# Kernel optimization log

Hardware: AMD Instinct MI355X
Metric: run time of the kernel (lower is better)

The kernel has to match this reference:

```python
import jax, jax.numpy as jnp
import numpy as np

DIM, M, K = 768, 48, 256
MK = M * K            # 12288
H = MK // 2           # 6144
MID = int(0.75 * MK)  # 9216
B = 2048
MIN_DIST_FACTOR = 10.0
LN_EPS = 1e-5


def setup_inputs() -> dict:
    key = jax.random.key(0)
    ks = jax.random.split(key, 18)
    s = 0.02  # keep exp(sigma_logits) tame
    return {
        "x": jax.random.normal(ks[0], (B, DIM), jnp.float32),
        "codebook": jax.random.normal(ks[1], (M, K, DIM // M), jnp.float32),
        "rot1": jnp.eye(DIM) + s * jax.random.normal(ks[2], (DIM, DIM), jnp.float32),
        "ln_g": jnp.ones((DIM,), jnp.float32),
        "ln_b": jnp.zeros((DIM,), jnp.float32),
        "l1_w": s * jax.random.normal(ks[3], (MID, DIM), jnp.float32),
        "l1_b": jnp.zeros((MID,), jnp.float32),
        "mu_w": s * jax.random.normal(ks[4], (H, MID), jnp.float32),
        "mu_b": jnp.zeros((H,), jnp.float32),
        "sig_w": s * jax.random.normal(ks[5], (H, MID), jnp.float32),
        "sig_b": jnp.zeros((H,), jnp.float32),
        "rot2": jnp.eye(H) + s * jax.random.normal(ks[6], (H, H), jnp.float32),
        "l2_w": s * jax.random.normal(ks[7], (MK, H), jnp.float32),
        "l2_b": jnp.zeros((MK,), jnp.float32),
        "interp_param": jax.random.normal(ks[8], (1,), jnp.float32),
        "vae_noise": jax.random.normal(ks[9], (B, H), jnp.float32),
        "gumbel_noise": -jnp.log(-jnp.log(
            jax.random.uniform(ks[10], (B, M, K), jnp.float32, 1e-10, 1.0))),
    }


def _layernorm(x, g, b):
    mu = jnp.mean(x, axis=-1, keepdims=True)
    var = jnp.mean((x - mu) ** 2, axis=-1, keepdims=True)
    return (x - mu) * jax.lax.rsqrt(var + LN_EPS) * g + b


def reference(x, codebook, rot1, ln_g, ln_b, l1_w, l1_b, mu_w, mu_b,
              sig_w, sig_b, rot2, l2_w, l2_b, interp_param,
              vae_noise, gumbel_noise):
    x_rot = x @ rot1.T                                   # [B, DIM]
    xn = _layernorm(x_rot, ln_g, ln_b)
    h1 = jax.nn.relu(xn @ l1_w.T + l1_b)                 # [B, MID]
    mu = h1 @ mu_w.T + mu_b                              # [B, H]
    sigma = jnp.exp(h1 @ sig_w.T + sig_b)                # [B, H]
    z = mu + sigma * vae_noise                           # reparameterized sample
    h = jnp.tanh(z)
    h_rot = h @ rot2.T                                   # [B, H]
    a = jax.nn.relu(h_rot @ l2_w.T + l2_b)               # [B, MK]
    a_r = a.reshape(-1, M, K)                            # [B, M, K]
    # PQ distances: [B, M, 1, d] vs [1, M, K, d] -> [B, M, K]
    d = DIM // M
    xs = x_rot.reshape(-1, M, 1, d)
    cs = codebook.reshape(1, M, K, d)
    dist = jnp.sum((cs - xs) ** 2, axis=-1)
    min_dist = jax.nn.one_hot(jnp.argmin(dist, axis=-1), K, dtype=jnp.float32)
    interp = jax.nn.sigmoid(interp_param[0])
    logits = (1.0 - interp) * a_r + interp * MIN_DIST_FACTOR * min_dist
    # hard gumbel-softmax, tau=1
    y_soft = jax.nn.softmax(logits + gumbel_noise, axis=-1)
    y_hard = jax.nn.one_hot(jnp.argmax(y_soft, axis=-1), K, dtype=y_soft.dtype)
    s = y_hard - jax.lax.stop_gradient(y_soft) + y_soft
    return s
```

## Files before the change

### kernel.cpp

```cpp
#include <hip/hip_runtime.h>
#include <cstddef>
#include <cstdint>

constexpr int kDIM = 768;
constexpr int kM   = 48;
constexpr int kK   = 256;
constexpr int kB   = 2048;
constexpr int kMID = 9216;
constexpr int kH   = 6144;
constexpr int kMK  = 12288;

using bf8v  = __attribute__((ext_vector_type(8))) short;
using f32x4 = __attribute__((ext_vector_type(4))) float;
using s8v   = __attribute__((ext_vector_type(8))) short;

template<bool HASBIAS, int EPI, typename OUT_T>
__global__ __launch_bounds__(256)
void gemm_nt_acc64(const float* __restrict__ A, const float* __restrict__ W,
                   const float* __restrict__ bias, OUT_T* C,
                   const float* zslog, const float* __restrict__ znoise,
                   int N, int Kd)
{
  __shared__ float As[16][132];
  __shared__ float Bs[16][132];
  const int tid  = (int)threadIdx.x;
  const int row0 = (int)blockIdx.y * 128;
  const int col0 = (int)blockIdx.x * 128;
  const int ty = tid >> 4, tx = tid & 15;
  const int i0 = ty * 8, j0 = tx * 8;
  const int fi1 = tid >> 2;
  const int fi2 = fi1 + 64;
  const int kc  = (tid & 3) * 4;

  const float* Ap1 = A + (size_t)(row0 + fi1) * Kd + kc;
  const float* Ap2 = A + (size_t)(row0 + fi2) * Kd + kc;
  const float* Wp1 = W + (size_t)(col0 + fi1) * Kd + kc;
  const float* Wp2 = W + (size_t)(col0 + fi2) * Kd + kc;

  double acc[8][8];
#pragma unroll
  for (int r = 0; r < 8; ++r)
#pragma unroll
    for (int c = 0; c < 8; ++c) acc[r][c] = 0.0;

  for (int kt = 0; kt < Kd; kt += 16) {
    const float4 a1 = *(const float4*)(Ap1 + kt);
    const float4 a2 = *(const float4*)(Ap2 + kt);
    const float4 b1 = *(const float4*)(Wp1 + kt);
    const float4 b2 = *(const float4*)(Wp2 + kt);
    As[kc + 0][fi1] = a1.x; As[kc + 1][fi1] = a1.y; As[kc + 2][fi1] = a1.z; As[kc + 3][fi1] = a1.w;
    As[kc + 0][fi2] = a2.x; As[kc + 1][fi2] = a2.y; As[kc + 2][fi2] = a2.z; As[kc + 3][fi2] = a2.w;
    Bs[kc + 0][fi1] = b1.x; Bs[kc + 1][fi1] = b1.y; Bs[kc + 2][fi1] = b1.z; Bs[kc + 3][fi1] = b1.w;
    Bs[kc + 0][fi2] = b2.x; Bs[kc + 1][fi2] = b2.y; Bs[kc + 2][fi2] = b2.z; Bs[kc + 3][fi2] = b2.w;
    __syncthreads();
#pragma unroll
    for (int kk = 0; kk < 16; ++kk) {
      const float4 av0 = *(const float4*)&As[kk][i0];
      const float4 av1 = *(const float4*)&As[kk][i0 + 4];
      const float4 bv0 = *(const float4*)&Bs[kk][j0];
      const float4 bv1 = *(const float4*)&Bs[kk][j0 + 4];
      const float ar[8] = {av0.x, av0.y, av0.z, av0.w, av1.x, av1.y, av1.z, av1.w};
      const float br[8] = {bv0.x, bv0.y, bv0.z, bv0.w, bv1.x, bv1.y, bv1.z, bv1.w};
      double bd[8];
#pragma unroll
      for (int c = 0; c < 8; ++c) bd[c] = (double)br[c];
#pragma unroll
      for (int r = 0; r < 8; ++r) {
        const double ad = (double)ar[r];
#pragma unroll
        for (int c = 0; c < 8; ++c)
          acc[r][c] = fma(ad, bd[c], acc[r][c]);
      }
    }
    __syncthreads();
  }

  double bvv[8];
#pragma unroll
  for (int c = 0; c < 8; ++c) bvv[c] = 0.0;
  if (HASBIAS) {
#pragma unroll
    for (int c = 0; c < 8; ++c) bvv[c] = (double)bias[col0 + j0 + c];
  }

#pragma unroll
  for (int r = 0; r < 8; ++r) {
    const size_t gbase = (size_t)(row0 + i0 + r) * N + col0 + j0;
    double o[8];
#pragma unroll
    for (int c = 0; c < 8; ++c) {
      double v = acc[r][c];
      if (HASBIAS) v += bvv[c];
      if (EPI == 1) v = fmax(v, 0.0);
      if (EPI == 2) {
        const double sg = exp((double)zslog[gbase + c]);
        v = tanh(v + sg * (double)znoise[gbase + c]);
      }
      o[c] = v;
    }
    if constexpr (sizeof(OUT_T) == 4) {
      float* dst = (float*)C + gbase;
      ((float4*)dst)[0] = make_float4((float)o[0], (float)o[1], (float)o[2], (float)o[3]);
      ((float4*)dst)[1] = make_float4((float)o[4], (float)o[5], (float)o[6], (float)o[7]);
    } else {
      double* dst = (double*)C + gbase;
#pragma unroll
      for (int c = 0; c < 8; ++c) dst[c] = o[c];
    }
  }
}

__device__ __forceinline__ unsigned short bf16rn(float f) {
  const unsigned u = __float_as_uint(f);
  return (unsigned short)((u + 0x7FFFu + ((u >> 16) & 1u)) >> 16);
}

__global__ __launch_bounds__(256)
void split3_k(const float* __restrict__ in, short* __restrict__ out, size_t n)
{
  const size_t i = ((size_t)blockIdx.x * 256 + threadIdx.x) * 8;
  const float4 v0 = *(const float4*)(in + i);
  const float4 v1 = *(const float4*)(in + i + 4);
  const float f[8] = {v0.x, v0.y, v0.z, v0.w, v1.x, v1.y, v1.z, v1.w};
  s8v o1, o2, o3;
#pragma unroll
  for (int j = 0; j < 8; ++j) {
    const unsigned short b1 = bf16rn(f[j]);
    const float r1 = f[j] - __uint_as_float((unsigned)b1 << 16);
    const unsigned short b2 = bf16rn(r1);
    const float r2 = r1 - __uint_as_float((unsigned)b2 << 16);
    const unsigned short b3 = bf16rn(r2);
    o1[j] = (short)b1; o2[j] = (short)b2; o3[j] = (short)b3;
  }
  *(s8v*)(out + i)         = o1;
  *(s8v*)(out + n + i)     = o2;
  *(s8v*)(out + 2 * n + i) = o3;
}

#define GLL16(SRC, DST) __builtin_amdgcn_global_load_lds( \
    (const __attribute__((address_space(1))) void*)(SRC), \
    (__attribute__((address_space(3))) void*)(DST), 16, 0, 0)

template<bool HASBIAS, bool RELU>
__global__ __launch_bounds__(256, 2)
void gemm3_bf16(const short* __restrict__ A3, const short* __restrict__ W3,
                const float* __restrict__ bias, float* __restrict__ C,
                int N, int Kd, int nbx)
{
  __shared__ short lds[6][4096];
  short* smem = &lds[0][0];
  const char* smemc = (const char*)smem;

  int wg = (int)blockIdx.x;
  const int nwg = (int)gridDim.x;
  if ((nwg & 7) == 0) { const int q = nwg >> 3; wg = (wg & 7) * q + (wg >> 3); }
  const int nby = kB / 128;
  const int by = wg % nby, bx = wg / nby;
  const int row0 = by * 128, col0 = bx * 128;

  const int tid = (int)threadIdx.x;
  const int l = tid & 63, w = tid >> 6;
  const int wr = (w & 1) * 64, wc = (w >> 1) * 64;

  const size_t planeAB = (size_t)2048 * Kd * 2;
  const size_t planeWB = (size_t)N * Kd * 2;
  const char* A3b = (const char*)A3;
  const char* W3b = (const char*)W3;

  const int su = 2 * w;
  const int r0 = su * 16 + (l >> 2), r1 = r0 + 16;
  const int q0 = (((l & 3) ^ (r0 & 3)) << 4);
  const int q1 = (((l & 3) ^ (r1 & 3)) << 4);
  const size_t offA0 = (size_t)(row0 + r0) * Kd * 2 + q0;
  const size_t offA1 = (size_t)(row0 + r1) * Kd * 2 + q1;
  const size_t offW0 = (size_t)(col0 + r0) * Kd * 2 + q0;
  const size_t offW1 = (size_t)(col0 + r1) * Kd * 2 + q1;
  short* dA0 = smem + (su + 0) * 512;
  short* dA1 = smem + (su + 1) * 512;

  int aoff[3][4], boff[3][4];
#pragma unroll
  for (int p = 0; p < 3; ++p) {
#pragma unroll
    for (int t = 0; t < 4; ++t) {
      const int Ra = wr + t * 16 + (l & 15);
      aoff[p][t] = p * 8192 + Ra * 64 + ((((l >> 4) << 4)) ^ ((Ra & 3) << 4));
      const int Rb = wc + t * 16 + (l & 15);
      boff[p][t] = (3 + p) * 8192 + Rb * 64 + ((((l >> 4) << 4)) ^ ((Rb & 3) << 4));
    }
  }

  f32x4 acc[4][4];
#pragma unroll
  for (int i = 0; i < 4; ++i)
#pragma unroll
    for (int j = 0; j < 4; ++j) acc[i][j] = f32x4{0.f, 0.f, 0.f, 0.f};

  for (int kt = 0; kt < Kd; kt += 32) {
    const size_t kb = (size_t)kt * 2;
#pragma unroll
    for (int t = 0; t < 3; ++t) {
      GLL16(A3b + t * planeAB + offA0 + kb, dA0 + t * 4096);
      GLL16(A3b + t * planeAB + offA1 + kb, dA1 + t * 4096);
    }
#pragma unroll
    for (int t = 0; t < 3; ++t) {
      GLL16(W3b + t * planeWB + offW0 + kb, dA0 + (3 + t) * 4096);
      GLL16(W3b + t * planeWB + offW1 + kb, dA1 + (3 + t) * 4096);
    }
    __syncthreads();

    bf8v af[3][4], bf_[3][4];
#pragma unroll
    for (int p = 0; p < 3; ++p)
#pragma unroll
      for (int t = 0; t < 4; ++t) {
        af[p][t]  = *(const bf8v*)(smemc + aoff[p][t]);
        bf_[p][t] = *(const bf8v*)(smemc + boff[p][t]);
      }
#pragma unroll
    for (int tr = 0; tr < 4; ++tr)
#pragma unroll
      for (int tc = 0; tc < 4; ++tc) {
        f32x4 c = acc[tr][tc];
        c = __builtin_amdgcn_mfma_f32_16x16x32_bf16(af[0][tr], bf_[0][tc], c, 0, 0, 0);
        c = __builtin_amdgcn_mfma_f32_16x16x32_bf16(af[0][tr], bf_[1][tc], c, 0, 0, 0);
        c = __builtin_amdgcn_mfma_f32_16x16x32_bf16(af[1][tr], bf_[0][tc], c, 0, 0, 0);
        c = __builtin_amdgcn_mfma_f32_16x16x32_bf16(af[0][tr], bf_[2][tc], c, 0, 0, 0);
        c = __builtin_amdgcn_mfma_f32_16x16x32_bf16(af[2][tr], bf_[0][tc], c, 0, 0, 0);
        c = __builtin_amdgcn_mfma_f32_16x16x32_bf16(af[1][tr], bf_[1][tc], c, 0, 0, 0);
        acc[tr][tc] = c;
      }
    __syncthreads();
  }

#pragma unroll
  for (int tc = 0; tc < 4; ++tc) {
    const int colg = col0 + wc + tc * 16 + (l & 15);
    float bv = 0.f;
    if (HASBIAS) bv = bias[colg];
#pragma unroll
    for (int tr = 0; tr < 4; ++tr) {
      const int rowg0 = row0 + wr + tr * 16 + ((l >> 4) << 2);
#pragma unroll
      for (int g = 0; g < 4; ++g) {
        float v = acc[tr][tc][g];
        if (HASBIAS) v += bv;
        if (RELU)    v = fmaxf(v, 0.f);
        C[(size_t)(rowg0 + g) * N + colg] = v;
      }
    }
  }
}

__global__ __launch_bounds__(256)
void layernorm_k(const double* __restrict__ in, const float* __restrict__ g,
                 const float* __restrict__ b, float* __restrict__ out)
{
  const int row = (int)blockIdx.x;
  const int tid = (int)threadIdx.x;
  const double* x = in + (size_t)row * kDIM;
  const double v0 = x[tid], v1 = x[tid + 256], v2 = x[tid + 512];
  __shared__ double red[8];
  double s = v0 + v1 + v2;
#pragma unroll
  for (int off = 32; off; off >>= 1) s += __shfl_xor(s, off);
  if ((tid & 63) == 0) red[tid >> 6] = s;
  __syncthreads();
  const double mean = (red[0] + red[1] + red[2] + red[3]) * (1.0 / 768.0);
  const double d0 = v0 - mean, d1 = v1 - mean, d2 = v2 - mean;
  double q = d0 * d0 + d1 * d1 + d2 * d2;
#pragma unroll
  for (int off = 32; off; off >>= 1) q += __shfl_xor(q, off);
  if ((tid & 63) == 0) red[4 + (tid >> 6)] = q;
  __syncthreads();
  const double var = (red[4] + red[5] + red[6] + red[7]) * (1.0 / 768.0);
  const double rs = 1.0 / sqrt(var + 1e-5);
  float* y = out + (size_t)row * kDIM;
  y[tid]       = (float)(d0 * rs * (double)g[tid]       + (double)b[tid]);
  y[tid + 256] = (float)(d1 * rs * (double)g[tid + 256] + (double)b[tid + 256]);
  y[tid + 512] = (float)(d2 * rs * (double)g[tid + 512] + (double)b[tid + 512]);
}

__global__ __launch_bounds__(256)
void zh_k(const float* __restrict__ mu, float* slog_h, const float* __restrict__ noise)
{
  const size_t i = (size_t)blockIdx.x * 256 + threadIdx.x;
  const double z = (double)mu[i] + exp((double)slog_h[i]) * (double)noise[i];
  slog_h[i] = (float)tanh(z);
}

__global__ __launch_bounds__(256)
void mindist_k(const double* __restrict__ xrot, const float* __restrict__ cb,
               int* __restrict__ minidx)
{
  const int wid  = (int)blockIdx.x * 4 + ((int)threadIdx.x >> 6);
  const int lane = (int)threadIdx.x & 63;
  const int bi = wid / kM, mi = wid % kM;
  const double* xv = xrot + (size_t)bi * kDIM + mi * 16;
  double xs[16];
#pragma unroll
  for (int d = 0; d < 16; ++d) xs[d] = xv[d];
  const float* cm = cb + (size_t)mi * (kK * 16);
  double best = 1e300; int bidx = 0;
#pragma unroll
  for (int j = 0; j < 4; ++j) {
    const int k = lane * 4 + j;
    const float* ck = cm + k * 16;
    double s = 0.0;
#pragma unroll
    for (int d = 0; d < 16; ++d) {
      const double t = (double)ck[d] - xs[d];
      s = fma(t, t, s);
    }
    if (s < best) { best = s; bidx = k; }
  }
#pragma unroll
  for (int off = 32; off; off >>= 1) {
    const double ob = __shfl_xor(best, off);
    const int    oi = __shfl_xor(bidx, off);
    if (ob < best || (ob == best && oi < bidx)) { best = ob; bidx = oi; }
  }
  if (lane == 0) minidx[wid] = bidx;
}

__global__ __launch_bounds__(256)
void finalize_k(float* a, const float* __restrict__ gumbel,
                const int* __restrict__ minidx, const float* __restrict__ interp_param)
{
  const int wid  = (int)blockIdx.x * 4 + ((int)threadIdx.x >> 6);
  const int lane = (int)threadIdx.x & 63;
  const double interp = 1.0 / (1.0 + exp(-(double)interp_param[0]));
  const double w = 1.0 - interp;
  const double bonus = interp * 10.0;
  const int mi = minidx[wid];
  const size_t base = (size_t)wid * 256 + lane * 4;
  const float4 av = *(const float4*)&a[base];
  const float4 gv = *(const float4*)&gumbel[base];
  const int k0 = lane * 4;
  double lg[4] = {w * (double)av.x + (double)gv.x,
                  w * (double)av.y + (double)gv.y,
                  w * (double)av.z + (double)gv.z,
                  w * (double)av.w + (double)gv.w};
#pragma unroll
  for (int j = 0; j < 4; ++j)
    if (k0 + j == mi) lg[j] += bonus;

  double best = -1e300; int bk = 0;
#pragma unroll
  for (int j = 0; j < 4; ++j)
    if (lg[j] > best) { best = lg[j]; bk = k0 + j; }
#pragma unroll
  for (int off = 32; off; off >>= 1) {
    const double ob = __shfl_xor(best, off);
    const int    oi = __shfl_xor(bk, off);
    if (ob > best || (ob == best && oi < bk)) { best = ob; bk = oi; }
  }
  float4 o;
  o.x = (k0 + 0 == bk) ? 1.f : 0.f;
  o.y = (k0 + 1 == bk) ? 1.f : 0.f;
  o.z = (k0 + 2 == bk) ? 1.f : 0.f;
  o.w = (k0 + 3 == bk) ? 1.f : 0.f;
  *(float4*)&a[base] = o;
}

extern "C" void kernel_launch(void* const* d_in, const int* in_sizes, int n_in,
                              void* d_out, int out_size, void* d_ws, size_t ws_size,
                              hipStream_t stream)
{
  const float* x      = (const float*)d_in[0];
  const float* cb     = (const float*)d_in[1];
  const float* rot1   = (const float*)d_in[2];
  const float* ln_g   = (const float*)d_in[3];
  const float* ln_b   = (const float*)d_in[4];
  const float* l1_w   = (const float*)d_in[5];
  const float* l1_b   = (const float*)d_in[6];
  const float* mu_w   = (const float*)d_in[7];
  const float* mu_b   = (const float*)d_in[8];
  const float* sig_w  = (const float*)d_in[9];
  const float* sig_b  = (const float*)d_in[10];
  const float* rot2   = (const float*)d_in[11];
  const float* l2_w   = (const float*)d_in[12];
  const float* l2_b   = (const float*)d_in[13];
  const float* interp = (const float*)d_in[14];
  const float* noise  = (const float*)d_in[15];
  const float* gumb   = (const float*)d_in[16];

  const dim3 blk(256);
  float* aout = (float*)d_out;

  const size_t nXrot = (size_t)kB * kDIM;
  const size_t nH1   = (size_t)kB * kMID;
  const size_t nHH   = (size_t)kB * kH;
  const size_t NEED  = nXrot * 8 + nXrot * 4 + nH1 * 4 + nHH * 4 + nHH * 4
                     + nH1 * 3 * 2 + (size_t)kMK * kH * 3 * 2 + (size_t)kB * kM * 4;

  if (ws_size >= NEED) {
    char* p = (char*)d_ws;
    double* x_rotd = (double*)p;              p += nXrot * 8;
    float*  xn     = (float*)p;               p += nXrot * 4;
    float*  h1     = (float*)p;               p += nH1 * 4;
    float*  mu     = (float*)p;               p += nHH * 4;
    float*  slog   = (float*)p;               p += nHH * 4;
    short*  As3    = (short*)p;               p += nH1 * 3 * 2;
    short*  Ws3    = (short*)p;               p += (size_t)kMK * kH * 3 * 2;
    int*    midx   = (int*)p;

    gemm_nt_acc64<false, 0, double><<<dim3(kDIM / 128, kB / 128), blk, 0, stream>>>(
        x, rot1, nullptr, x_rotd, nullptr, nullptr, kDIM, kDIM);
    layernorm_k<<<dim3(kB), blk, 0, stream>>>(x_rotd, ln_g, ln_b, xn);
    mindist_k<<<dim3(kB * kM / 4), blk, 0, stream>>>(x_rotd, cb, midx);

    split3_k<<<dim3((unsigned)(nXrot / 2048)), blk, 0, stream>>>(xn, As3, nXrot);
    split3_k<<<dim3((unsigned)((size_t)kMID * kDIM / 2048)), blk, 0, stream>>>(l1_w, Ws3, (size_t)kMID * kDIM);
    gemm3_bf16<true, true><<<dim3(kMID / 128 * (kB / 128)), blk, 0, stream>>>(
        As3, Ws3, l1_b, h1, kMID, kDIM, kMID / 128);

    split3_k<<<dim3((unsigned)(nH1 / 2048)), blk, 0, stream>>>(h1, As3, nH1);
    split3_k<<<dim3((unsigned)((size_t)kH * kMID / 2048)), blk, 0, stream>>>(mu_w, Ws3, (size_t)kH * kMID);
    gemm3_bf16<true, false><<<dim3(kH / 128 * (kB / 128)), blk, 0, stream>>>(
        As3, Ws3, mu_b, mu, kH, kMID, kH / 128);
    split3_k<<<dim3((unsigned)((size_t)kH * kMID / 2048)), blk, 0, stream>>>(sig_w, Ws3, (size_t)kH * kMID);
    gemm3_bf16<true, false><<<dim3(kH / 128 * (kB / 128)), blk, 0, stream>>>(
        As3, Ws3, sig_b, slog, kH, kMID, kH / 128);

    zh_k<<<dim3((unsigned)(nHH / 256)), blk, 0, stream>>>(mu, slog, noise);

    split3_k<<<dim3((unsigned)(nHH / 2048)), blk, 0, stream>>>(slog, As3, nHH);
    split3_k<<<dim3((unsigned)((size_t)kH * kH / 2048)), blk, 0, stream>>>(rot2, Ws3, (size_t)kH * kH);
    gemm3_bf16<false, false><<<dim3(kH / 128 * (kB / 128)), blk, 0, stream>>>(
        As3, Ws3, nullptr, h1, kH, kH, kH / 128);

    split3_k<<<dim3((unsigned)(nHH / 2048)), blk, 0, stream>>>(h1, As3, nHH);
    split3_k<<<dim3((unsigned)((size_t)kMK * kH / 2048)), blk, 0, stream>>>(l2_w, Ws3, (size_t)kMK * kH);
    gemm3_bf16<true, true><<<dim3(kMK / 128 * (kB / 128)), blk, 0, stream>>>(
        As3, Ws3, l2_b, aout, kMK, kH, kMK / 128);

    finalize_k<<<dim3(kB * kM / 4), blk, 0, stream>>>(aout, gumb, midx, interp);
    return;
  }

  char* wsb    = (char*)d_ws;
  double* x_rotd = (double*)wsb;
  float*  xn     = (float*)(wsb + (size_t)kB * kDIM * 8);
  float*  h1     = xn   + (size_t)kB * kDIM;
  float*  slog   = h1   + (size_t)kB * kMID;
  int*    midx   = (int*)(slog + (size_t)kB * kH);
  float*  hrot   = h1;

  gemm_nt_acc64<false, 0, double><<<dim3(kDIM / 128, kB / 128), blk, 0, stream>>>(
      x, rot1, nullptr, x_rotd, nullptr, nullptr, kDIM, kDIM);
  layernorm_k<<<dim3(kB), blk, 0, stream>>>(x_rotd, ln_g, ln_b, xn);
  mindist_k<<<dim3(kB * kM / 4), blk, 0, stream>>>(x_rotd, cb, midx);
  gemm_nt_acc64<true, 1, float><<<dim3(kMID / 128, kB / 128), blk, 0, stream>>>(
      xn, l1_w, l1_b, h1, nullptr, nullptr, kMID, kDIM);
  gemm_nt_acc64<true, 0, float><<<dim3(kH / 128, kB / 128), blk, 0, stream>>>(
      h1, sig_w, sig_b, slog, nullptr, nullptr, kH, kMID);
  gemm_nt_acc64<true, 2, float><<<dim3(kH / 128, kB / 128), blk, 0, stream>>>(
      h1, mu_w, mu_b, slog, slog, noise, kH, kMID);
  gemm_nt_acc64<false, 0, float><<<dim3(kH / 128, kB / 128), blk, 0, stream>>>(
      slog, rot2, nullptr, hrot, nullptr, nullptr, kH, kH);
  gemm_nt_acc64<true, 1, float><<<dim3(kMK / 128, kB / 128), blk, 0, stream>>>(
      hrot, l2_w, l2_b, aout, nullptr, nullptr, kMK, kH);
  finalize_k<<<dim3(kB * kM / 4), blk, 0, stream>>>(aout, gumb, midx, interp);
}
```

Before: 6.455 ms.

## Double-buffer LDS tiles in split-bf16 GEMM to overlap loads with MFMA

The split-bf16 GEMM now keeps two LDS stages and issues the global-to-LDS loads for the next K-step before running the MFMAs on the current stage. It waits with an explicit vmcnt(0) and a barrier at the end of each iteration, replacing the load-then-sync-then-compute pattern. The LDS swizzle is also changed so the row-dependent XOR uses bits 1-2 of the row. The point is to hide global load latency behind compute. The cost is 96KB of LDS per block, which likely limits occupancy to one block per CU, and the launch-bounds occupancy hint is dropped.

```diff
diff --git a/kernel.cpp b/kernel.cpp
--- a/kernel.cpp
+++ b/kernel.cpp
@@ -13,6 +13,13 @@
 using bf8v  = __attribute__((ext_vector_type(8))) short;
 using f32x4 = __attribute__((ext_vector_type(4))) float;
 using s8v   = __attribute__((ext_vector_type(8))) short;
+
+#define GLL16(SRC, DST) __builtin_amdgcn_global_load_lds( \
+    (const __attribute__((address_space(1))) void*)(SRC), \
+    (__attribute__((address_space(3))) void*)(DST), 16, 0, 0)
+
+#define FENCE() asm volatile("" ::: "memory")
+#define WAITV0() asm volatile("s_waitcnt vmcnt(0)" ::: "memory")
 
 template<bool HASBIAS, int EPI, typename OUT_T>
 __global__ __launch_bounds__(256)
@@ -137,19 +144,13 @@
   *(s8v*)(out + 2 * n + i) = o3;
 }
 
-#define GLL16(SRC, DST) __builtin_amdgcn_global_load_lds( \
-    (const __attribute__((address_space(1))) void*)(SRC), \
-    (__attribute__((address_space(3))) void*)(DST), 16, 0, 0)
-
 template<bool HASBIAS, bool RELU>
-__global__ __launch_bounds__(256, 2)
+__global__ __launch_bounds__(256)
 void gemm3_bf16(const short* __restrict__ A3, const short* __restrict__ W3,
                 const float* __restrict__ bias, float* __restrict__ C,
                 int N, int Kd, int nbx)
 {
-  __shared__ short lds[6][4096];
-  short* smem = &lds[0][0];
-  const char* smemc = (const char*)smem;
+  __shared__ char ldsb[98304];
 
   int wg = (int)blockIdx.x;
   const int nwg = (int)gridDim.x;
@@ -169,14 +170,13 @@
 
   const int su = 2 * w;
   const int r0 = su * 16 + (l >> 2), r1 = r0 + 16;
-  const int q0 = (((l & 3) ^ (r0 & 3)) << 4);
-  const int q1 = (((l & 3) ^ (r1 & 3)) << 4);
-  const size_t offA0 = (size_t)(row0 + r0) * Kd * 2 + q0;
-  const size_t offA1 = (size_t)(row0 + r1) * Kd * 2 + q1;
-  const size_t offW0 = (size_t)(col0 + r0) * Kd * 2 + q0;
-  const size_t offW1 = (size_t)(col0 + r1) * Kd * 2 + q1;
-  short* dA0 = smem + (su + 0) * 512;
-  short* dA1 = smem + (su + 1) * 512;
+  const int qsw = (((l & 3) ^ ((l >> 3) & 3)) << 4);
+  const size_t offA0 = (size_t)(row0 + r0) * Kd * 2 + qsw;
+  const size_t offA1 = (size_t)(row0 + r1) * Kd * 2 + qsw;
+  const size_t offW0 = (size_t)(col0 + r0) * Kd * 2 + qsw;
+  const size_t offW1 = (size_t)(col0 + r1) * Kd * 2 + qsw;
+  const int d0 = su * 1024;
+  const int d1 = d0 + 1024;
 
   int aoff[3][4], boff[3][4];
 #pragma unroll
@@ -184,9 +184,9 @@
 #pragma unroll
     for (int t = 0; t < 4; ++t) {
       const int Ra = wr + t * 16 + (l & 15);
-      aoff[p][t] = p * 8192 + Ra * 64 + ((((l >> 4) << 4)) ^ ((Ra & 3) << 4));
+      aoff[p][t] = p * 8192 + Ra * 64 + ((((l >> 4)) ^ ((Ra >> 1) & 3)) << 4);
       const int Rb = wc + t * 16 + (l & 15);
-      boff[p][t] = (3 + p) * 8192 + Rb * 64 + ((((l >> 4) << 4)) ^ ((Rb & 3) << 4));
+      boff[p][t] = (3 + p) * 8192 + Rb * 64 + ((((l >> 4)) ^ ((Rb >> 1) & 3)) << 4);
     }
   }
 
@@ -196,27 +196,43 @@
 #pragma unroll
     for (int j = 0; j < 4; ++j) acc[i][j] = f32x4{0.f, 0.f, 0.f, 0.f};
 
-  for (int kt = 0; kt < Kd; kt += 32) {
-    const size_t kb = (size_t)kt * 2;
+  const int NITER = Kd >> 5;
+
+  {
+    char* nb = ldsb;
 #pragma unroll
     for (int t = 0; t < 3; ++t) {
-      GLL16(A3b + t * planeAB + offA0 + kb, dA0 + t * 4096);
-      GLL16(A3b + t * planeAB + offA1 + kb, dA1 + t * 4096);
-    }
-#pragma unroll
-    for (int t = 0; t < 3; ++t) {
-      GLL16(W3b + t * planeWB + offW0 + kb, dA0 + (3 + t) * 4096);
-      GLL16(W3b + t * planeWB + offW1 + kb, dA1 + (3 + t) * 4096);
-    }
-    __syncthreads();
+      GLL16(A3b + t * planeAB + offA0, nb + t * 8192 + d0);
+      GLL16(A3b + t * planeAB + offA1, nb + t * 8192 + d1);
+      GLL16(W3b + t * planeWB + offW0, nb + (3 + t) * 8192 + d0);
+      GLL16(W3b + t * planeWB + offW1, nb + (3 + t) * 8192 + d1);
+    }
+  }
+  FENCE(); WAITV0(); __builtin_amdgcn_s_barrier(); FENCE();
+
+  for (int it = 0; it < NITER; ++it) {
+    const int par = it & 1;
+    const char* base = ldsb + par * 49152;
+
+    if (it + 1 < NITER) {
+      const size_t kb = (size_t)(it + 1) * 64;
+      char* nb = ldsb + (par ^ 1) * 49152;
+#pragma unroll
+      for (int t = 0; t < 3; ++t) {
+        GLL16(A3b + t * planeAB + offA0 + kb, nb + t * 8192 + d0);
+        GLL16(A3b + t * planeAB + offA1 + kb, nb + t * 8192 + d1);
+        GLL16(W3b + t * planeWB + offW0 + kb, nb + (3 + t) * 8192 + d0);
+        GLL16(W3b + t * planeWB + offW1 + kb, nb + (3 + t) * 8192 + d1);
+      }
+    }
 
     bf8v af[3][4], bf_[3][4];
 #pragma unroll
     for (int p = 0; p < 3; ++p)
 #pragma unroll
       for (int t = 0; t < 4; ++t) {
-        af[p][t]  = *(const bf8v*)(smemc + aoff[p][t]);
-        bf_[p][t] = *(const bf8v*)(smemc + boff[p][t]);
+        af[p][t]  = *(const bf8v*)(base + aoff[p][t]);
+        bf_[p][t] = *(const bf8v*)(base + boff[p][t]);
       }
 #pragma unroll
     for (int tr = 0; tr < 4; ++tr)
@@ -231,7 +247,8 @@
         c = __builtin_amdgcn_mfma_f32_16x16x32_bf16(af[1][tr], bf_[1][tc], c, 0, 0, 0);
         acc[tr][tc] = c;
       }
-    __syncthreads();
+
+    FENCE(); WAITV0(); __builtin_amdgcn_s_barrier(); FENCE();
   }
 
 #pragma unroll
```

After: 7.017 ms. +8.7%, slower.
